# Optimization experiments

Hardware: AMD Instinct MI355X
Metric: run time of the kernel (lower is better)

## Reference

```python
import jax, jax.numpy as jnp
import numpy as np

N_VIEWS = 2
TEMPERATURE = 0.07


def setup_inputs() -> dict:
    key = jax.random.key(0)
    # concatenated features for n_views=2 views of batch_size=4096, proj dim 128
    features = jax.random.normal(key, (8192, 128), dtype=jnp.float32)
    return {"features": features}


def reference(features) -> jnp.ndarray:
    # NT-Xent / SimCLR loss, faithful to the torch module:
    #   sim = F F^T ; drop diagonal ; logits = [positive, negatives] / T ;
    #   CE with label 0  ==  mean( logsumexp(off_diag/T) - positive/T )
    # (concatenating [pos, neg] is a row permutation of the off-diagonal
    #  entries, and CrossEntropy(label=0) only needs logsumexp(row) - pos.)
    N = features.shape[0]
    B = N // N_VIEWS
    inv_t = 1.0 / TEMPERATURE

    sim = jnp.matmul(features, features.T)  # [N, N]

    row = jnp.arange(N)
    # off-diagonal column indices in increasing-j order, matching mask.view:
    # cols[i] = [0..i-1, i+1..N-1]
    cols = jnp.arange(N - 1)[None, :]
    cols = cols + (cols >= row[:, None])  # [N, N-1]
    sim_offdiag = jnp.take_along_axis(sim, cols, axis=1)  # [N, N-1]

    # with n_views=2 the single positive for row i is its other view (i+B) % N
    pos = sim[row, (row + B) % N]  # [N]

    lse = jax.nn.logsumexp(sim_offdiag * inv_t, axis=1)  # [N]
    loss = jnp.mean(lse - pos * inv_t)
    return loss
```

## Files before the change

### kernel.cpp

```cpp
#include <hip/hip_runtime.h>
#include <math.h>

typedef __bf16 bf16x8 __attribute__((ext_vector_type(8)));
typedef float f32x4 __attribute__((ext_vector_type(4)));
typedef unsigned short u16x8 __attribute__((ext_vector_type(8)));

#define N_TOT 8192
#define HALF_N 4096
#define D 128
#define INV_T 14.285714285714286f
#define CSC 20.609929155556627f
#define NCSC -20.609929155556627f
#define LN2F 0.69314718055994531f
#define NEG_BIG -3.0e38f
#define M_INIT -1.0e30f
#define THR_RAW 1.0f
#define CS 16

__device__ __forceinline__ unsigned short f2bf(float f) {
    union { float f; unsigned int u; } a; a.f = f;
    unsigned int u = a.u;
    return (unsigned short)((u + 0x7fffu + ((u >> 16) & 1u)) >> 16);
}

__global__ __launch_bounds__(256)
void cvt_kernel(const float* __restrict__ in, unsigned short* __restrict__ fbP) {
    const int c   = blockIdx.x * 256 + threadIdx.x;
    const int q   = c >> 6;
    const int rem = c & 63;
    const int lg  = rem >> 4, lr = rem & 15;
    const int kk  = q & 3;
    const int col = (q >> 2) * 16 + lr;
    const int j16 = kk * 4 + lg;
    const float4 v0 = reinterpret_cast<const float4*>(in)[col * 32 + j16 * 2];
    const float4 v1 = reinterpret_cast<const float4*>(in)[col * 32 + j16 * 2 + 1];
    u16x8 o;
    o[0] = f2bf(v0.x); o[1] = f2bf(v0.y); o[2] = f2bf(v0.z); o[3] = f2bf(v0.w);
    o[4] = f2bf(v1.x); o[5] = f2bf(v1.y); o[6] = f2bf(v1.z); o[7] = f2bf(v1.w);
    reinterpret_cast<u16x8*>(fbP)[c] = o;
}

__global__ __launch_bounds__(512, 4)
void simclr_kernel(const unsigned short* __restrict__ fbP,
                   float* __restrict__ pm, float* __restrict__ ps,
                   float* __restrict__ rowpos) {
    const int tid  = threadIdx.x;
    const int lane = tid & 63;
    const int wid  = tid >> 6;
    const int lr   = lane & 15;
    const int lg   = lane >> 4;
    const int RT0  = blockIdx.x * 16 + wid * 2;
    const int Tw   = blockIdx.y * 32;

    auto ld16 = [&](int chunk) -> bf16x8 {
        return *reinterpret_cast<const bf16x8*>(fbP + (size_t)chunk * 8);
    };

    bf16x8 br[2][4];
#pragma unroll
    for (int rt = 0; rt < 2; ++rt)
#pragma unroll
        for (int kk = 0; kk < 4; ++kk)
            br[rt][kk] = ld16(((RT0 + rt) * 4 + kk) * 64 + lane);

    float m[2], s[2];
#pragma unroll
    for (int rt = 0; rt < 2; ++rt) { m[rt] = M_INIT; s[rt] = 0.f; }

    bf16x8 ca[4], cb[4];
#pragma unroll
    for (int kk = 0; kk < 4; ++kk) ca[kk] = ld16((Tw * 4 + kk) * 64 + lane);
#pragma unroll
    for (int kk = 0; kk < 4; ++kk) cb[kk] = ld16(((Tw + 1) * 4 + kk) * 64 + lane);

#pragma unroll 1
    for (int i = 0; i < 16; ++i) {
        const int c0 = blockIdx.y * 512 + i * 32;

        f32x4 accP[2], accQ[2];
#pragma unroll
        for (int rt = 0; rt < 2; ++rt) accP[rt] = f32x4{0.f, 0.f, 0.f, 0.f};
#pragma unroll
        for (int kk = 0; kk < 4; ++kk)
#pragma unroll
            for (int rt = 0; rt < 2; ++rt)
                accP[rt] = __builtin_amdgcn_mfma_f32_16x16x32_bf16(ca[kk], br[rt][kk], accP[rt], 0, 0, 0);
        if (i < 15) {
#pragma unroll
            for (int kk = 0; kk < 4; ++kk)
                ca[kk] = ld16(((Tw + 2 * i + 2) * 4 + kk) * 64 + lane);
        }

#pragma unroll
        for (int rt = 0; rt < 2; ++rt) accQ[rt] = f32x4{0.f, 0.f, 0.f, 0.f};
#pragma unroll
        for (int kk = 0; kk < 4; ++kk)
#pragma unroll
            for (int rt = 0; rt < 2; ++rt)
                accQ[rt] = __builtin_amdgcn_mfma_f32_16x16x32_bf16(cb[kk], br[rt][kk], accQ[rt], 0, 0, 0);
        if (i < 15) {
#pragma unroll
            for (int kk = 0; kk < 4; ++kk)
                cb[kk] = ld16(((Tw + 2 * i + 3) * 4 + kk) * 64 + lane);
        }

#pragma unroll
        for (int rt = 0; rt < 2; ++rt) {
            const int rowbase = (RT0 + rt) * 16;
            f32x4 P = accP[rt], Q = accQ[rt];
            if (c0 == (rowbase ^ HALF_N)) {
#pragma unroll
                for (int r = 0; r < 4; ++r)
                    if (lr == lg * 4 + r) rowpos[rowbase + lr] = P[r];
            }
            if (c0 + 16 == (rowbase ^ HALF_N)) {
#pragma unroll
                for (int r = 0; r < 4; ++r)
                    if (lr == lg * 4 + r) rowpos[rowbase + lr] = Q[r];
            }
            if (c0 == rowbase) {
#pragma unroll
                for (int r = 0; r < 4; ++r)
                    if (lr == lg * 4 + r) P[r] = NEG_BIG;
            }
            if (c0 + 16 == rowbase) {
#pragma unroll
                for (int r = 0; r < 4; ++r)
                    if (lr == lg * 4 + r) Q[r] = NEG_BIG;
            }
            const float t1 = fmaxf(fmaxf(P[0], P[1]), P[2]);
            const float t2 = fmaxf(fmaxf(P[3], Q[0]), Q[1]);
            const float t3 = fmaxf(Q[2], Q[3]);
            const float rmax = fmaxf(fmaxf(t1, t2), t3);
            if (!__all(rmax <= m[rt] + THR_RAW)) {
                const float mn = fmaxf(m[rt], rmax);
                s[rt] *= __builtin_amdgcn_exp2f(fmaf(m[rt], CSC, mn * NCSC));
                m[rt] = mn;
            }
            const float cm = m[rt] * NCSC;
            const float e0 = __builtin_amdgcn_exp2f(fmaf(P[0], CSC, cm));
            const float e1 = __builtin_amdgcn_exp2f(fmaf(P[1], CSC, cm));
            const float e2 = __builtin_amdgcn_exp2f(fmaf(P[2], CSC, cm));
            const float e3 = __builtin_amdgcn_exp2f(fmaf(P[3], CSC, cm));
            const float e4 = __builtin_amdgcn_exp2f(fmaf(Q[0], CSC, cm));
            const float e5 = __builtin_amdgcn_exp2f(fmaf(Q[1], CSC, cm));
            const float e6 = __builtin_amdgcn_exp2f(fmaf(Q[2], CSC, cm));
            const float e7 = __builtin_amdgcn_exp2f(fmaf(Q[3], CSC, cm));
            s[rt] += ((e0 + e1) + (e2 + e3)) + ((e4 + e5) + (e6 + e7));
        }
    }

#pragma unroll
    for (int rt = 0; rt < 2; ++rt) {
        float M = m[rt];
        M = fmaxf(M, __shfl_xor(M, 16, 64));
        M = fmaxf(M, __shfl_xor(M, 32, 64));
        float sc = s[rt] * __builtin_amdgcn_exp2f(fmaf(m[rt], CSC, M * NCSC));
        sc += __shfl_xor(sc, 16, 64);
        sc += __shfl_xor(sc, 32, 64);
        if (lg == 0) {
            const int row = (RT0 + rt) * 16 + lr;
            pm[blockIdx.y * N_TOT + row] = M;
            ps[blockIdx.y * N_TOT + row] = sc;
        }
    }
}

__global__ __launch_bounds__(256)
void rowloss_kernel(const float* __restrict__ pm, const float* __restrict__ ps,
                    const float* __restrict__ rowpos, float* __restrict__ rowloss) {
    const int row = blockIdx.x * 256 + threadIdx.x;
    float M = pm[row], S = ps[row];
#pragma unroll
    for (int c = 1; c < CS; ++c) {
        const float Mo = pm[c * N_TOT + row], So = ps[c * N_TOT + row];
        const float mn = fmaxf(M, Mo);
        S = fmaf(S,  __builtin_amdgcn_exp2f(fmaf(M,  CSC, mn * NCSC)),
                 So * __builtin_amdgcn_exp2f(fmaf(Mo, CSC, mn * NCSC)));
        M = mn;
    }
    rowloss[row] = LN2F * fmaf(M, CSC, __builtin_amdgcn_logf(S)) - rowpos[row] * INV_T;
}

__global__ __launch_bounds__(256)
void mean_kernel(const float* __restrict__ rowloss, float* __restrict__ out) {
    float acc = 0.f;
    for (int i = threadIdx.x; i < N_TOT; i += 256) acc += rowloss[i];
#pragma unroll
    for (int off = 32; off > 0; off >>= 1) acc += __shfl_xor(acc, off, 64);
    __shared__ float ls[4];
    if ((threadIdx.x & 63) == 0) ls[threadIdx.x >> 6] = acc;
    __syncthreads();
    if (threadIdx.x == 0)
        out[0] = (ls[0] + ls[1] + ls[2] + ls[3]) * (1.0f / (float)N_TOT);
}

extern "C" void kernel_launch(void* const* d_in, const int* in_sizes, int n_in,
                              void* d_out, int out_size, void* d_ws, size_t ws_size,
                              hipStream_t stream) {
    const float* feat = (const float*)d_in[0];
    char* ws = (char*)d_ws;
    unsigned short* fbP = (unsigned short*)ws;
    float* pm      = (float*)(ws + (size_t)N_TOT * D * 2);
    float* ps      = (float*)(ws + (size_t)N_TOT * D * 2 + (size_t)CS * N_TOT * 4);
    float* rowpos  = (float*)(ws + (size_t)N_TOT * D * 2 + 2 * (size_t)CS * N_TOT * 4);
    float* rowloss = (float*)(ws + (size_t)N_TOT * D * 2 + 2 * (size_t)CS * N_TOT * 4 + N_TOT * 4);
    float* out = (float*)d_out;

    cvt_kernel<<<512, 256, 0, stream>>>(feat, fbP);
    simclr_kernel<<<dim3(32, CS), 512, 0, stream>>>(fbP, pm, ps, rowpos);
    rowloss_kernel<<<N_TOT / 256, 256, 0, stream>>>(pm, ps, rowpos, rowloss);
    mean_kernel<<<1, 256, 0, stream>>>(rowloss, out);
}
```

Before: 45.34 us.

## Stagger column-tile order per wave, raise MFMA priority, fuse rowloss and mean

Each wave now starts its walk over column tiles at a different offset, so waves in a block read different tiles of the packed features at the same moment. The MFMA sections are wrapped in s_setprio so matrix work is issued ahead of other instructions. The rowloss and mean kernels are merged into one kernel that reduces within each block and atomically adds into the output, which is zeroed by a memset first. This drops one launch and the rowloss buffer, but the final sum order now depends on atomic ordering, so the result is no longer bit-deterministic.

```diff
diff --git a/kernel.cpp b/kernel.cpp
--- a/kernel.cpp
+++ b/kernel.cpp
@@ -67,41 +67,47 @@
 #pragma unroll
     for (int rt = 0; rt < 2; ++rt) { m[rt] = M_INIT; s[rt] = 0.f; }
 
+    int p = (wid & 3) << 2;
     bf16x8 ca[4], cb[4];
 #pragma unroll
-    for (int kk = 0; kk < 4; ++kk) ca[kk] = ld16((Tw * 4 + kk) * 64 + lane);
-#pragma unroll
-    for (int kk = 0; kk < 4; ++kk) cb[kk] = ld16(((Tw + 1) * 4 + kk) * 64 + lane);
+    for (int kk = 0; kk < 4; ++kk) ca[kk] = ld16(((Tw + 2 * p) * 4 + kk) * 64 + lane);
+#pragma unroll
+    for (int kk = 0; kk < 4; ++kk) cb[kk] = ld16(((Tw + 2 * p + 1) * 4 + kk) * 64 + lane);
 
 #pragma unroll 1
     for (int i = 0; i < 16; ++i) {
-        const int c0 = blockIdx.y * 512 + i * 32;
+        const int pn = (p + 1) & 15;
+        const int c0 = blockIdx.y * 512 + p * 32;
 
         f32x4 accP[2], accQ[2];
 #pragma unroll
         for (int rt = 0; rt < 2; ++rt) accP[rt] = f32x4{0.f, 0.f, 0.f, 0.f};
+        __builtin_amdgcn_s_setprio(1);
 #pragma unroll
         for (int kk = 0; kk < 4; ++kk)
 #pragma unroll
             for (int rt = 0; rt < 2; ++rt)
                 accP[rt] = __builtin_amdgcn_mfma_f32_16x16x32_bf16(ca[kk], br[rt][kk], accP[rt], 0, 0, 0);
+        __builtin_amdgcn_s_setprio(0);
         if (i < 15) {
 #pragma unroll
             for (int kk = 0; kk < 4; ++kk)
-                ca[kk] = ld16(((Tw + 2 * i + 2) * 4 + kk) * 64 + lane);
+                ca[kk] = ld16(((Tw + 2 * pn) * 4 + kk) * 64 + lane);
         }
 
 #pragma unroll
         for (int rt = 0; rt < 2; ++rt) accQ[rt] = f32x4{0.f, 0.f, 0.f, 0.f};
+        __builtin_amdgcn_s_setprio(1);
 #pragma unroll
         for (int kk = 0; kk < 4; ++kk)
 #pragma unroll
             for (int rt = 0; rt < 2; ++rt)
                 accQ[rt] = __builtin_amdgcn_mfma_f32_16x16x32_bf16(cb[kk], br[rt][kk], accQ[rt], 0, 0, 0);
+        __builtin_amdgcn_s_setprio(0);
         if (i < 15) {
 #pragma unroll
             for (int kk = 0; kk < 4; ++kk)
-                cb[kk] = ld16(((Tw + 2 * i + 3) * 4 + kk) * 64 + lane);
+                cb[kk] = ld16(((Tw + 2 * pn + 1) * 4 + kk) * 64 + lane);
         }
 
 #pragma unroll
@@ -148,6 +154,7 @@
             const float e7 = __builtin_amdgcn_exp2f(fmaf(Q[3], CSC, cm));
             s[rt] += ((e0 + e1) + (e2 + e3)) + ((e4 + e5) + (e6 + e7));
         }
+        p = pn;
     }
 
 #pragma unroll
@@ -167,8 +174,8 @@
 }
 
 __global__ __launch_bounds__(256)
-void rowloss_kernel(const float* __restrict__ pm, const float* __restrict__ ps,
-                    const float* __restrict__ rowpos, float* __restrict__ rowloss) {
+void rowloss_mean_kernel(const float* __restrict__ pm, const float* __restrict__ ps,
+                         const float* __restrict__ rowpos, float* __restrict__ out) {
     const int row = blockIdx.x * 256 + threadIdx.x;
     float M = pm[row], S = ps[row];
 #pragma unroll
@@ -179,20 +186,14 @@
                  So * __builtin_amdgcn_exp2f(fmaf(Mo, CSC, mn * NCSC)));
         M = mn;
     }
-    rowloss[row] = LN2F * fmaf(M, CSC, __builtin_amdgcn_logf(S)) - rowpos[row] * INV_T;
-}
-
-__global__ __launch_bounds__(256)
-void mean_kernel(const float* __restrict__ rowloss, float* __restrict__ out) {
-    float acc = 0.f;
-    for (int i = threadIdx.x; i < N_TOT; i += 256) acc += rowloss[i];
+    float acc = LN2F * fmaf(M, CSC, __builtin_amdgcn_logf(S)) - rowpos[row] * INV_T;
 #pragma unroll
     for (int off = 32; off > 0; off >>= 1) acc += __shfl_xor(acc, off, 64);
     __shared__ float ls[4];
     if ((threadIdx.x & 63) == 0) ls[threadIdx.x >> 6] = acc;
     __syncthreads();
     if (threadIdx.x == 0)
-        out[0] = (ls[0] + ls[1] + ls[2] + ls[3]) * (1.0f / (float)N_TOT);
+        atomicAdd(out, (ls[0] + ls[1] + ls[2] + ls[3]) * (1.0f / (float)N_TOT));
 }
 
 extern "C" void kernel_launch(void* const* d_in, const int* in_sizes, int n_in,
@@ -204,11 +205,10 @@
     float* pm      = (float*)(ws + (size_t)N_TOT * D * 2);
     float* ps      = (float*)(ws + (size_t)N_TOT * D * 2 + (size_t)CS * N_TOT * 4);
     float* rowpos  = (float*)(ws + (size_t)N_TOT * D * 2 + 2 * (size_t)CS * N_TOT * 4);
-    float* rowloss = (float*)(ws + (size_t)N_TOT * D * 2 + 2 * (size_t)CS * N_TOT * 4 + N_TOT * 4);
     float* out = (float*)d_out;
 
+    hipMemsetAsync(out, 0, sizeof(float), stream);
     cvt_kernel<<<512, 256, 0, stream>>>(feat, fbP);
     simclr_kernel<<<dim3(32, CS), 512, 0, stream>>>(fbP, pm, ps, rowpos);
-    rowloss_kernel<<<N_TOT / 256, 256, 0, stream>>>(pm, ps, rowpos, rowloss);
-    mean_kernel<<<1, 256, 0, stream>>>(rowloss, out);
-}
+    rowloss_mean_kernel<<<N_TOT / 256, 256, 0, stream>>>(pm, ps, rowpos, out);
+}
```

New measurement: 43.92 us. 3.1% less time.
